# Kernel tuning notes

Measured on AMD Instinct MI355X. Metric: run time of the kernel, lower is better.

The kernel has to match this reference:

```python
import jax, jax.numpy as jnp
import numpy as np

DIM = 16
NUM_SPECIES = 10
CUTOFF = 5.0
NUM_CONVS = 3
N_ATM = 131072
N_BND = 1048576
N_ANG = 2097152
N_GRAPHS = 256
PI = 3.141592653589793


def _bessel(x, end, num_basis):
    # Sinusoidal (Bessel) radial basis on (0, end]. x: [E] -> [E, num_basis]
    xx = x[:, None] + 1e-5
    n = jnp.arange(1, num_basis + 1, dtype=x.dtype)
    return jnp.sqrt(2.0 / end) * jnp.sin(n * PI * xx / end) / xx


def _gaussian(x, start, end, num_basis):
    centers = jnp.linspace(start, end, num_basis).astype(x.dtype)
    gamma = 1.0 / (centers[1] - centers[0])
    return jnp.exp(-(gamma * (x[:, None] - centers)) ** 2)


def _ln(x, g, b):
    mu = jnp.mean(x, -1, keepdims=True)
    var = jnp.var(x, -1, keepdims=True)
    return (x - mu) * jax.lax.rsqrt(var + 1e-5) * g + b


def _embed(feat, W1, b1, W2, b2, g, b):
    # MLP([in, dim, dim], SiLU) + LayerNorm
    h = jax.nn.silu(feat @ W1 + b1)
    return _ln(h @ W2 + b2, g, b)


def _egconv(x, e, src, dst, W, bvec, lnp):
    # Edge-gated graph convolution (ALIGNN layer).
    # W: [5, D, D] = (W_src, W_dst, W_e, W_self, W_nbr); bvec: [2, D]; lnp: [2, 2, D]
    z = x[src] @ W[0] + x[dst] @ W[1] + e @ W[2] + bvec[0]  # [E, D]
    sigma = jax.nn.sigmoid(z)
    msg = sigma * (x[src] @ W[4])
    num = jax.ops.segment_sum(msg, dst, num_segments=x.shape[0])
    den = jax.ops.segment_sum(sigma, dst, num_segments=x.shape[0])
    x_new = x + jax.nn.silu(_ln(x @ W[3] + bvec[1] + num / (den + 1e-5), lnp[0, 0], lnp[0, 1]))
    e_new = e + jax.nn.silu(_ln(z, lnp[1, 0], lnp[1, 1]))
    return x_new, e_new


def _forward(x_atm, x_bnd, x_ang, mask_dih_ang, edge_index_G, edge_index_A, x_atm_batch,
             forcepair, enc_W1, enc_b1, enc_W2, enc_b2, enc_ln_g, enc_ln_b,
             conv_W, conv_b, conv_ln, l1_W, l1_b, l2_W, l2_b):
    # ---- Encoder ----
    # atom species one-hot, zero-padded from NUM_SPECIES to DIM columns (extra W rows unused)
    atm_feat = jax.nn.one_hot(x_atm, DIM, dtype=enc_W1.dtype)
    h_atm = _embed(atm_feat, enc_W1[0], enc_b1[0], enc_W2[0], enc_b2[0], enc_ln_g[0], enc_ln_b[0])
    h_bnd = _embed(_bessel(x_bnd, CUTOFF, DIM), enc_W1[1], enc_b1[1], enc_W2[1], enc_b2[1], enc_ln_g[1], enc_ln_b[1])
    h_ang_b = _embed(_gaussian(x_ang, 0.0, PI, DIM), enc_W1[2], enc_b1[2], enc_W2[2], enc_b2[2], enc_ln_g[2], enc_ln_b[2])
    h_ang_d = _embed(_gaussian(x_ang, -PI, PI, DIM), enc_W1[3], enc_b1[3], enc_W2[3], enc_b2[3], enc_ln_g[3], enc_ln_b[3])
    h_ang = jnp.where(mask_dih_ang[:, None], h_ang_d, h_ang_b)  # dihedral=True branch
    # ---- Processor: interleaved line-graph / atom-graph edge-gated convs ----
    srcA, dstA = edge_index_A[0], edge_index_A[1]
    srcG, dstG = edge_index_G[0], edge_index_G[1]
    for c in range(NUM_CONVS):
        h_bnd, h_ang = _egconv(h_bnd, h_ang, srcA, dstA, conv_W[c, 0], conv_b[c, 0], conv_ln[c, 0])
        h_atm, h_bnd = _egconv(h_atm, h_bnd, srcG, dstG, conv_W[c, 1], conv_b[c, 1], conv_ln[c, 1])
    # ---- Decoder: sum-pool atoms per graph ----
    h_pooled = jax.ops.segment_sum(h_atm, x_atm_batch, num_segments=N_GRAPHS)  # [G, D]
    # ---- Head ----
    x = jnp.concatenate([h_pooled, forcepair.reshape(N_GRAPHS, 2)], axis=-1)  # [G, D+2]
    x = jax.nn.leaky_relu(x @ l1_W + l1_b, negative_slope=0.01)
    return x @ l2_W + l2_b  # [G, 1]


def setup_inputs() -> dict:
    key = jax.random.key(0)
    ks = jax.random.split(key, 16)
    f32 = jnp.float32
    s = 0.25
    inp = {}
    inp["x_atm"] = jax.random.randint(ks[0], (N_ATM,), 0, NUM_SPECIES)
    inp["x_bnd"] = jax.random.uniform(ks[1], (N_BND,), f32, 0.5, CUTOFF)
    inp["x_ang"] = jax.random.uniform(ks[2], (N_ANG,), f32, -PI, PI)
    inp["mask_dih_ang"] = jax.random.randint(ks[3], (N_ANG,), 0, 2).astype(bool)
    inp["edge_index_G"] = jax.random.randint(ks[4], (2, N_BND), 0, N_ATM)
    inp["edge_index_A"] = jax.random.randint(ks[5], (2, N_ANG), 0, N_BND)
    inp["x_atm_batch"] = jnp.sort(jax.random.randint(ks[6], (N_ATM,), 0, N_GRAPHS))
    inp["forcepair"] = jax.random.normal(ks[7], (N_GRAPHS * 2,), f32)
    inp["enc_W1"] = jax.random.normal(ks[8], (4, DIM, DIM), f32) * s
    inp["enc_b1"] = jnp.zeros((4, DIM), f32)
    inp["enc_W2"] = jax.random.normal(ks[9], (4, DIM, DIM), f32) * s
    inp["enc_b2"] = jnp.zeros((4, DIM), f32)
    inp["enc_ln_g"] = jnp.ones((4, DIM), f32)
    inp["enc_ln_b"] = jnp.zeros((4, DIM), f32)
    inp["conv_W"] = jax.random.normal(ks[10], (NUM_CONVS, 2, 5, DIM, DIM), f32) * s
    inp["conv_b"] = jnp.zeros((NUM_CONVS, 2, 2, DIM), f32)
    inp["conv_ln"] = jnp.stack([jnp.ones((NUM_CONVS, 2, 2, DIM), f32), jnp.zeros((NUM_CONVS, 2, 2, DIM), f32)], axis=3)  # [C,2,2(node/edge? no: gamma/beta at axis 3)] -> [C,2,2,2,D]
    inp["l1_W"] = jax.random.normal(ks[11], (DIM + 2, DIM), f32) * s
    inp["l1_b"] = jnp.zeros((DIM,), f32)
    inp["l2_W"] = jax.random.normal(ks[12], (DIM, 1), f32) * s
    inp["l2_b"] = jnp.zeros((1,), f32)
    return inp


def reference(x_atm, x_bnd, x_ang, mask_dih_ang, edge_index_G, edge_index_A, x_atm_batch,
              forcepair, enc_W1, enc_b1, enc_W2, enc_b2, enc_ln_g, enc_ln_b,
              conv_W, conv_b, conv_ln, l1_W, l1_b, l2_W, l2_b):
    return _forward(x_atm, x_bnd, x_ang, mask_dih_ang, edge_index_G, edge_index_A, x_atm_batch,
                    forcepair, enc_W1, enc_b1, enc_W2, enc_b2, enc_ln_g, enc_ln_b,
                    conv_W, conv_b, conv_ln, l1_W, l1_b, l2_W, l2_b)
```

## Files before the change

kernel.cpp:

```cpp
#include <hip/hip_runtime.h>
#include <hip/hip_bf16.h>

#define N_ATM 131072
#define N_BND 1048576
#define N_ANG 2097152
#define N_GRAPHS 256
#define D_SPLIT (N_BND / 2)
#define CAP_SLOTS (N_ANG / 2 + 16384)
#define PI_F 3.14159265358979323846f

typedef __hip_bfloat16 bf16;

__device__ __forceinline__ int clampi(int v, int lo, int hi) {
    return v < lo ? lo : (v > hi ? hi : v);
}
__device__ __forceinline__ float b2f(bf16 v) { return __bfloat162float(v); }
__device__ __forceinline__ float sigmoidf_(float x) { return 1.0f / (1.0f + __expf(-x)); }
__device__ __forceinline__ float siluf_(float x) { return x / (1.0f + __expf(-x)); }

__device__ __forceinline__ float loadF(const void* p, long long i, int isbf) {
    return isbf ? b2f(((const bf16*)p)[i]) : ((const float*)p)[i];
}
__device__ __forceinline__ float bfbits2f(unsigned lo16) {
    union { unsigned u; float f; } c; c.u = lo16 << 16; return c.f;
}
__device__ __forceinline__ unsigned f2bfbits(float f) {
    union { float f; unsigned u; } c; c.f = f;
    unsigned u = c.u + 0x7FFFu + ((c.u >> 16) & 1u);
    return u >> 16;
}

__device__ __forceinline__ void load16b(const bf16* p, float* r) {
    uint4 a = ((const uint4*)p)[0];
    uint4 b = ((const uint4*)p)[1];
    unsigned w[8] = {a.x, a.y, a.z, a.w, b.x, b.y, b.z, b.w};
#pragma unroll
    for (int i = 0; i < 8; i++) {
        r[2*i] = bfbits2f(w[i] & 0xFFFFu);
        union { unsigned u; float f; } c; c.u = w[i] & 0xFFFF0000u;
        r[2*i+1] = c.f;
    }
}
__device__ __forceinline__ void store16b(bf16* p, const float* r) {
    unsigned w[8];
#pragma unroll
    for (int i = 0; i < 8; i++)
        w[i] = f2bfbits(r[2*i]) | (f2bfbits(r[2*i+1]) << 16);
    ((uint4*)p)[0] = make_uint4(w[0], w[1], w[2], w[3]);
    ((uint4*)p)[1] = make_uint4(w[4], w[5], w[6], w[7]);
}

__global__ void __launch_bounds__(256) k_zero_int(int* __restrict__ p, int n) {
    int i = blockIdx.x * 256 + threadIdx.x;
    if (i < n) p[i] = 0;
}

__global__ void __launch_bounds__(256) k_detect(const void* lng, const unsigned* __restrict__ mask,
                                                int* flags) {
    int i = blockIdx.x * 256 + threadIdx.x;
    if (i == 0) flags[0] = (*(const unsigned*)lng == 0x3F803F80u) ? 1 : 0;
    int bad = 0;
    for (int j = i; j < 512 * 1024; j += 512 * 256)
        if (mask[j] > 1u) bad = 1;
    if (bad) atomicOr(&flags[1], 1);
}

__global__ void k_cvt_any(const void* __restrict__ src, float* __restrict__ dst, int n,
                          const int* __restrict__ flags) {
    int i = blockIdx.x * blockDim.x + threadIdx.x;
    if (i < n) dst[i] = loadF(src, i, flags[0]);
}

__global__ void __launch_bounds__(256) k_count(const int* __restrict__ dst, int* __restrict__ cnt,
                                               int E, int n) {
    int i = blockIdx.x * 256 + threadIdx.x;
    if (i >= E) return;
    atomicAdd(&cnt[clampi(dst[i], 0, n - 1)], 1);
}
__global__ void __launch_bounds__(256) k_scan_local(const int* __restrict__ cnt, int* __restrict__ ofs,
                                                    int* __restrict__ bsum, int n) {
    __shared__ int s[256];
    int t = threadIdx.x, i = blockIdx.x * 256 + t;
    int v = (i < n) ? cnt[i] : 0;
    s[t] = v; __syncthreads();
    for (int o = 1; o < 256; o <<= 1) {
        int add = (t >= o) ? s[t - o] : 0;
        __syncthreads();
        s[t] += add;
        __syncthreads();
    }
    if (i < n) ofs[i] = s[t] - v;
    if (t == 255) bsum[blockIdx.x] = s[255];
}
__global__ void __launch_bounds__(256) k_scan_bsum(int* __restrict__ bsum, int nb) {
    __shared__ int s[256];
    __shared__ int run;
    int t = threadIdx.x;
    if (t == 0) run = 0;
    __syncthreads();
    for (int base = 0; base < nb; base += 256) {
        int i = base + t;
        int v = (i < nb) ? bsum[i] : 0;
        s[t] = v; __syncthreads();
        for (int o = 1; o < 256; o <<= 1) {
            int add = (t >= o) ? s[t - o] : 0;
            __syncthreads();
            s[t] += add;
            __syncthreads();
        }
        if (i < nb) bsum[i] = run + s[t] - v;
        __syncthreads();
        if (t == 0) run += s[255];
        __syncthreads();
    }
}
__global__ void __launch_bounds__(256) k_scan_add(int* __restrict__ ofs, const int* __restrict__ bsum,
                                                  int* __restrict__ cursor, int n) {
    int i = blockIdx.x * 256 + threadIdx.x;
    if (i < n) { int v = ofs[i] + bsum[blockIdx.x]; ofs[i] = v; cursor[i] = v; }
}
__global__ void __launch_bounds__(256) k_scatter_line(
    const int* __restrict__ src, const int* __restrict__ dst, int* __restrict__ cur,
    int* __restrict__ srcP, int* __restrict__ dstP, int* __restrict__ pos, int E, int n)
{
    int i = blockIdx.x * 256 + threadIdx.x;
    if (i >= E) return;
    int d = clampi(dst[i], 0, n - 1);
    int s = clampi(src[i], 0, n - 1);
    int p = clampi(atomicAdd(&cur[d], 1), 0, E - 1);
    srcP[p] = s; dstP[p] = d; pos[i] = p;
}
__global__ void __launch_bounds__(256) k_scatter_pos(
    const int* __restrict__ dst, int* __restrict__ cur, int* __restrict__ pos, int E, int n)
{
    int i = blockIdx.x * 256 + threadIdx.x;
    if (i >= E) return;
    int d = clampi(dst[i], 0, n - 1);
    pos[i] = clampi(atomicAdd(&cur[d], 1), 0, E - 1);
}

__global__ void __launch_bounds__(256) k_enc_atm(
    const int* __restrict__ sp_in,
    const void* W1, const void* b1, const void* W2, const void* b2,
    const void* g, const void* be, const int* __restrict__ flags,
    bf16* __restrict__ out)
{
    __shared__ float sW1[256], sW2[256], sb1[16], sb2[16], sg[16], sbe[16];
    int t = threadIdx.x, isbf = flags[0];
    sW1[t] = loadF(W1, t, isbf); sW2[t] = loadF(W2, t, isbf);
    if (t < 16) { sb1[t]=loadF(b1,t,isbf); sb2[t]=loadF(b2,t,isbf); sg[t]=loadF(g,t,isbf); sbe[t]=loadF(be,t,isbf); }
    __syncthreads();
    int i = blockIdx.x * 256 + t;
    if (i >= N_ATM) return;
    int sp = clampi(sp_in[i], 0, 15);
    float h[16];
#pragma unroll
    for (int j = 0; j < 16; j++) h[j] = siluf_(sW1[sp * 16 + j] + sb1[j]);
    float o[16]; float mu = 0.f;
#pragma unroll
    for (int j = 0; j < 16; j++) {
        float a = sb2[j];
#pragma unroll
        for (int k = 0; k < 16; k++) a += h[k] * sW2[k * 16 + j];
        o[j] = a; mu += a;
    }
    mu *= (1.f / 16.f);
    float var = 0.f;
#pragma unroll
    for (int j = 0; j < 16; j++) { float d = o[j] - mu; var += d * d; }
    var *= (1.f / 16.f);
    float r = rsqrtf(var + 1e-5f);
    float ov[16];
#pragma unroll
    for (int j = 0; j < 16; j++) ov[j] = (o[j] - mu) * r * sg[j] + sbe[j];
    store16b(out + (long long)i * 16, ov);
}

__global__ void __launch_bounds__(256) k_enc_bnd(
    const void* __restrict__ xb,
    const void* W1, const void* b1, const void* W2, const void* b2,
    const void* g, const void* be, const int* __restrict__ flags,
    bf16* __restrict__ out)
{
    __shared__ float sW1[256], sW2[256], sb1[16], sb2[16], sg[16], sbe[16];
    int t = threadIdx.x, isbf = flags[0];
    sW1[t] = loadF(W1, 256 + t, isbf); sW2[t] = loadF(W2, 256 + t, isbf);
    if (t < 16) { sb1[t]=loadF(b1,16+t,isbf); sb2[t]=loadF(b2,16+t,isbf); sg[t]=loadF(g,16+t,isbf); sbe[t]=loadF(be,16+t,isbf); }
    __syncthreads();
    int i = blockIdx.x * 256 + t;
    if (i >= N_BND) return;
    float x = loadF(xb, i, isbf) + 1e-5f;
    const float c = 0.6324555320336759f;
    float inv = c / x;
    float feat[16];
#pragma unroll
    for (int k = 0; k < 16; k++) feat[k] = __sinf((float)(k + 1) * PI_F * x * 0.2f) * inv;
    float h[16];
#pragma unroll
    for (int j = 0; j < 16; j++) {
        float a = sb1[j];
#pragma unroll
        for (int k = 0; k < 16; k++) a += feat[k] * sW1[k * 16 + j];
        h[j] = siluf_(a);
    }
    float o[16]; float mu = 0.f;
#pragma unroll
    for (int j = 0; j < 16; j++) {
        float a = sb2[j];
#pragma unroll
        for (int k = 0; k < 16; k++) a += h[k] * sW2[k * 16 + j];
        o[j] = a; mu += a;
    }
    mu *= (1.f / 16.f);
    float var = 0.f;
#pragma unroll
    for (int j = 0; j < 16; j++) { float d = o[j] - mu; var += d * d; }
    var *= (1.f / 16.f);
    float r = rsqrtf(var + 1e-5f);
    float ov[16];
#pragma unroll
    for (int j = 0; j < 16; j++) ov[j] = (o[j] - mu) * r * sg[j] + sbe[j];
    store16b(out + (long long)i * 16, ov);
}

__global__ void __launch_bounds__(256) k_enc_ang(
    const void* __restrict__ xa, const void* __restrict__ mask,
    const void* W1, const void* b1, const void* W2, const void* b2,
    const void* g, const void* be, const int* __restrict__ flags,
    const int* __restrict__ pos, bf16* __restrict__ out)
{
    __shared__ float sW1[512], sW2[512], sb1[32], sb2[32], sg[32], sbe[32];
    int t = threadIdx.x, isbf = flags[0], mbyte = flags[1];
    for (int i = t; i < 512; i += 256) { sW1[i] = loadF(W1, 512 + i, isbf); sW2[i] = loadF(W2, 512 + i, isbf); }
    if (t < 32) { sb1[t]=loadF(b1,32+t,isbf); sb2[t]=loadF(b2,32+t,isbf); sg[t]=loadF(g,32+t,isbf); sbe[t]=loadF(be,32+t,isbf); }
    __syncthreads();
    int i = blockIdx.x * 256 + t;
    if (i >= N_ANG) return;
    int m = mbyte ? (((const unsigned char*)mask)[i] != 0) : (((const int*)mask)[i] != 0);
    float x = loadF(xa, i, isbf);
    float gam = m ? 2.3873241463784303f : 4.7746482927568605f;
    float c0  = m ? -PI_F : 0.0f;
    float dc  = m ? 0.41887902047863906f : 0.20943951023931953f;
    int wo = m * 256, vo = m * 16;
    float feat[16];
#pragma unroll
    for (int k = 0; k < 16; k++) {
        float d = gam * (x - (c0 + (float)k * dc));
        feat[k] = __expf(-d * d);
    }
    float h[16];
#pragma unroll
    for (int j = 0; j < 16; j++) {
        float a = sb1[vo + j];
#pragma unroll
        for (int k = 0; k < 16; k++) a += feat[k] * sW1[wo + k * 16 + j];
        h[j] = siluf_(a);
    }
    float o[16]; float mu = 0.f;
#pragma unroll
    for (int j = 0; j < 16; j++) {
        float a = sb2[vo + j];
#pragma unroll
        for (int k = 0; k < 16; k++) a += h[k] * sW2[wo + k * 16 + j];
        o[j] = a; mu += a;
    }
    mu *= (1.f / 16.f);
    float var = 0.f;
#pragma unroll
    for (int j = 0; j < 16; j++) { float d = o[j] - mu; var += d * d; }
    var *= (1.f / 16.f);
    float r = rsqrtf(var + 1e-5f);
    float ov[16];
#pragma unroll
    for (int j = 0; j < 16; j++) ov[j] = (o[j] - mu) * r * sg[vo + j] + sbe[vo + j];
    store16b(out + (long long)clampi(pos[i], 0, N_ANG - 1) * 16, ov);
}

__device__ __forceinline__ void edge_core(
    const float* xs, const float* xd, const float* ev,
    const float* sW, const float* sB, const float* sLg, const float* sLb,
    float* eo, unsigned* wpk)
{
    float z[16], mm[16];
#pragma unroll
    for (int j = 0; j < 16; j++) { z[j] = sB[j]; mm[j] = 0.f; }
#pragma unroll
    for (int k = 0; k < 16; k++) {
        float a = xs[k], c = xd[k], q = ev[k];
#pragma unroll
        for (int j = 0; j < 16; j++) {
            z[j] += a * sW[k * 16 + j] + c * sW[256 + k * 16 + j] + q * sW[512 + k * 16 + j];
            mm[j] += a * sW[1024 + k * 16 + j];
        }
    }
    float mu = 0.f;
#pragma unroll
    for (int j = 0; j < 16; j++) mu += z[j];
    mu *= (1.f / 16.f);
    float var = 0.f;
#pragma unroll
    for (int j = 0; j < 16; j++) { float dd = z[j] - mu; var += dd * dd; }
    var *= (1.f / 16.f);
    float r = rsqrtf(var + 1e-5f);
#pragma unroll
    for (int j = 0; j < 16; j++)
        eo[j] = ev[j] + siluf_((z[j] - mu) * r * sLg[j] + sLb[j]);
#pragma unroll
    for (int i = 0; i < 8; i++) {
        float a0 = sigmoidf_(z[2*i]);
        float a1 = sigmoidf_(z[2*i+1]);
        wpk[i]     = f2bfbits(a0 * mm[2*i]) | (f2bfbits(a1 * mm[2*i+1]) << 16);
        wpk[8 + i] = f2bfbits(a0)           | (f2bfbits(a1) << 16);
    }
}

__global__ void __launch_bounds__(256) k_econv_side(
    const bf16* __restrict__ x, bf16* __restrict__ e,
    const int* __restrict__ srcP, const int* __restrict__ dstP,
    const float* __restrict__ W, const float* __restrict__ B, const float* __restrict__ L,
    bf16* __restrict__ scratch, int side, int E, int nn)
{
    __shared__ float sW[1280], sB[16], sLg[16], sLb[16];
    int t = threadIdx.x;
    for (int i = t; i < 1280; i += 256) sW[i] = W[i];
    if (t < 16) { sB[t] = B[t]; sLg[t] = L[32 + t]; sLb[t] = L[48 + t]; }
    __syncthreads();
    int p = blockIdx.x * 256 + t;
    if (p >= E) return;
    int d = clampi(dstP[p], 0, nn - 1);
    bool mine = side ? (d >= D_SPLIT) : (d < D_SPLIT);
    if (!mine) return;
    int s = clampi(srcP[p], 0, nn - 1);
    float xs[16], xd[16], ev[16];
    load16b(x + (long long)s * 16, xs);
    load16b(x + (long long)d * 16, xd);
    load16b(e + (long long)p * 16, ev);
    float eo[16]; unsigned wpk[16];
    edge_core(xs, xd, ev, sW, sB, sLg, sLb, eo, wpk);
    store16b(e + (long long)p * 16, eo);
    int slot = side ? (E - 1 - p) : p;
    slot = clampi(slot, 0, CAP_SLOTS - 1);
    uint4* sp4 = (uint4*)(scratch + (long long)slot * 32);
    sp4[0] = make_uint4(wpk[0],  wpk[1],  wpk[2],  wpk[3]);
    sp4[1] = make_uint4(wpk[4],  wpk[5],  wpk[6],  wpk[7]);
    sp4[2] = make_uint4(wpk[8],  wpk[9],  wpk[10], wpk[11]);
    sp4[3] = make_uint4(wpk[12], wpk[13], wpk[14], wpk[15]);
}

__global__ void __launch_bounds__(256) k_econv_nat(
    const bf16* __restrict__ x, bf16* __restrict__ e,
    const int* __restrict__ src, const int* __restrict__ dst, const int* __restrict__ pos,
    const float* __restrict__ W, const float* __restrict__ B, const float* __restrict__ L,
    bf16* __restrict__ scratch, int E, int nn)
{
    __shared__ float sW[1280], sB[16], sLg[16], sLb[16];
    int t = threadIdx.x;
    for (int i = t; i < 1280; i += 256) sW[i] = W[i];
    if (t < 16) { sB[t] = B[t]; sLg[t] = L[32 + t]; sLb[t] = L[48 + t]; }
    __syncthreads();
    int i = blockIdx.x * 256 + t;
    if (i >= E) return;
    int s = clampi(src[i], 0, nn - 1);
    int d = clampi(dst[i], 0, nn - 1);
    float xs[16], xd[16], ev[16];
    load16b(x + (long long)s * 16, xs);
    load16b(x + (long long)d * 16, xd);
    load16b(e + (long long)i * 16, ev);
    float eo[16]; unsigned wpk[16];
    edge_core(xs, xd, ev, sW, sB, sLg, sLb, eo, wpk);
    store16b(e + (long long)i * 16, eo);
    int slot = clampi(pos[i], 0, E - 1);
    uint4* sp4 = (uint4*)(scratch + (long long)slot * 32);
    sp4[0] = make_uint4(wpk[0],  wpk[1],  wpk[2],  wpk[3]);
    sp4[1] = make_uint4(wpk[4],  wpk[5],  wpk[6],  wpk[7]);
    sp4[2] = make_uint4(wpk[8],  wpk[9],  wpk[10], wpk[11]);
    sp4[3] = make_uint4(wpk[12], wpk[13], wpk[14], wpk[15]);
}

__global__ void __launch_bounds__(256) k_nconv(
    const bf16* __restrict__ xo, bf16* __restrict__ xn,
    const int* __restrict__ ofs, const int* __restrict__ endo,
    const float* __restrict__ W, const float* __restrict__ B, const float* __restrict__ L,
    const bf16* __restrict__ scratch, int mulp, int addc,
    int dlo, int dhi, int Emax, int cap)
{
    __shared__ float sW[256], sB[16], sLg[16], sLb[16];
    int t = threadIdx.x;
    sW[t] = W[768 + t];
    if (t < 16) { sB[t] = B[16 + t]; sLg[t] = L[t]; sLb[t] = L[16 + t]; }
    __syncthreads();
    int d = dlo + blockIdx.x * 256 + t;
    if (d >= dhi) return;
    float xv[16];
    load16b(xo + (long long)d * 16, xv);
    float num[16], den[16];
#pragma unroll
    for (int j = 0; j < 16; j++) { num[j] = 0.f; den[j] = 0.f; }
    int p0 = clampi(ofs[d], 0, Emax);
    int p1 = clampi(endo[d], p0, Emax);
    for (int p = p0; p < p1; p++) {
        int idx = clampi(mulp * p + addc, 0, cap - 1);
        const uint4* q = (const uint4*)(scratch + (long long)idx * 32);
        uint4 q0 = q[0], q1 = q[1], q2 = q[2], q3 = q[3];
        unsigned w[16] = {q0.x,q0.y,q0.z,q0.w, q1.x,q1.y,q1.z,q1.w,
                          q2.x,q2.y,q2.z,q2.w, q3.x,q3.y,q3.z,q3.w};
#pragma unroll
        for (int i = 0; i < 8; i++) {
            num[2*i]   += bfbits2f(w[i] & 0xFFFFu);
            num[2*i+1] += bfbits2f(w[i] >> 16);
            den[2*i]   += bfbits2f(w[8+i] & 0xFFFFu);
            den[2*i+1] += bfbits2f(w[8+i] >> 16);
        }
    }
    float tt[16]; float mu = 0.f;
#pragma unroll
    for (int j = 0; j < 16; j++) {
        float a = sB[j] + num[j] / (den[j] + 1e-5f);
#pragma unroll
        for (int k = 0; k < 16; k++) a += xv[k] * sW[k * 16 + j];
        tt[j] = a; mu += a;
    }
    mu *= (1.f / 16.f);
    float var = 0.f;
#pragma unroll
    for (int j = 0; j < 16; j++) { float dd = tt[j] - mu; var += dd * dd; }
    var *= (1.f / 16.f);
    float r = rsqrtf(var + 1e-5f);
    float ov[16];
#pragma unroll
    for (int j = 0; j < 16; j++)
        ov[j] = xv[j] + siluf_((tt[j] - mu) * r * sLg[j] + sLb[j]);
    store16b(xn + (long long)d * 16, ov);
}

__global__ void __launch_bounds__(256) k_pool2(
    const bf16* __restrict__ h, const int* __restrict__ batch, float* __restrict__ pooled)
{
    int g = blockIdx.x;
    int lo = 0, hi = N_ATM;
    while (lo < hi) { int m = (lo + hi) >> 1; if (batch[m] < g) lo = m + 1; else hi = m; }
    int s0 = lo;
    lo = 0; hi = N_ATM;
    while (lo < hi) { int m = (lo + hi) >> 1; if (batch[m] < g + 1) lo = m + 1; else hi = m; }
    int s1 = lo;
    float acc[16];
#pragma unroll
    for (int j = 0; j < 16; j++) acc[j] = 0.f;
    for (int i = s0 + threadIdx.x; i < s1; i += 256) {
        float v[16];
        load16b(h + (long long)i * 16, v);
#pragma unroll
        for (int j = 0; j < 16; j++) acc[j] += v[j];
    }
#pragma unroll
    for (int j = 0; j < 16; j++)
        for (int o = 32; o > 0; o >>= 1) acc[j] += __shfl_down(acc[j], o, 64);
    __shared__ float red[4][16];
    int wv = threadIdx.x >> 6, ln = threadIdx.x & 63;
    if (ln == 0)
#pragma unroll
        for (int j = 0; j < 16; j++) red[wv][j] = acc[j];
    __syncthreads();
    if (threadIdx.x < 16)
        pooled[g * 16 + threadIdx.x] = red[0][threadIdx.x] + red[1][threadIdx.x]
                                     + red[2][threadIdx.x] + red[3][threadIdx.x];
}

__global__ void __launch_bounds__(256) k_head(
    const float* __restrict__ pooled, const void* __restrict__ fp,
    const void* l1W, const void* l1b, const void* l2W, const void* l2b,
    const int* __restrict__ flags, void* __restrict__ out)
{
    __shared__ float sW[18 * 16], sb[16], s2W[16];
    int t = threadIdx.x, isbf = flags[0];
    for (int i = t; i < 288; i += 256) sW[i] = loadF(l1W, i, isbf);
    if (t < 16) { sb[t] = loadF(l1b, t, isbf); s2W[t] = loadF(l2W, t, isbf); }
    __syncthreads();
    int g = t;
    if (g >= N_GRAPHS) return;
    float in[18];
#pragma unroll
    for (int j = 0; j < 16; j++) in[j] = pooled[g * 16 + j];
    in[16] = loadF(fp, 2 * g, isbf);
    in[17] = loadF(fp, 2 * g + 1, isbf);
    float acc = loadF(l2b, 0, isbf);
#pragma unroll
    for (int j = 0; j < 16; j++) {
        float h = sb[j];
#pragma unroll
        for (int k = 0; k < 18; k++) h += in[k] * sW[k * 16 + j];
        h = (h > 0.f) ? h : 0.01f * h;
        acc += h * s2W[j];
    }
    if (isbf) ((bf16*)out)[g] = __float2bfloat16(acc);
    else      ((float*)out)[g] = acc;
}

extern "C" void kernel_launch(void* const* d_in, const int* in_sizes, int n_in,
                              void* d_out, int out_size, void* d_ws, size_t ws_size,
                              hipStream_t stream) {
    const int*  x_atm = (const int*)d_in[0];
    const void* x_bnd = d_in[1];
    const void* x_ang = d_in[2];
    const void* mask  = d_in[3];
    const int*  eiG   = (const int*)d_in[4];
    const int*  eiA   = (const int*)d_in[5];
    const int*  batch = (const int*)d_in[6];
    const void* fp    = d_in[7];
    const void* eW1 = d_in[8],  *eb1 = d_in[9],  *eW2 = d_in[10], *eb2 = d_in[11];
    const void* elg = d_in[12], *elb = d_in[13];
    const void* convW = d_in[14], *convB = d_in[15], *convLN = d_in[16];
    const void* l1W = d_in[17], *l1b = d_in[18], *l2W = d_in[19], *l2b = d_in[20];

    const size_t NA16 = (size_t)N_ATM * 16;
    const size_t NB16 = (size_t)N_BND * 16;
    const size_t NG16 = (size_t)N_ANG * 16;

    char* p = (char*)d_ws;
    int*   flags  = (int*)p;   p += 256;
    float* cw     = (float*)p; p += 7680 * 4;
    float* cb     = (float*)p; p += 192 * 4;
    float* cln    = (float*)p; p += 384 * 4;
    float* pooled = (float*)p; p += 4096 * 4;
    int*   bsum   = (int*)p;   p += 4096 * 4;
    int*   cntB   = (int*)p;   p += (size_t)N_BND * 4;
    int*   ofsB   = (int*)p;   p += (size_t)N_BND * 4;
    int*   srcB   = (int*)p;   p += (size_t)N_ANG * 4;
    int*   dstB   = (int*)p;   p += (size_t)N_ANG * 4;
    int*   cntA   = (int*)p;   p += (size_t)N_ATM * 4;
    int*   ofsA   = (int*)p;   p += (size_t)N_ATM * 4;
    int*   posG   = (int*)p;   p += (size_t)N_BND * 4;
    bf16*  h_atm  = (bf16*)p;  p += NA16 * 2;
    bf16*  h_bndX = (bf16*)p;  p += NB16 * 2;
    bf16*  h_bndY = (bf16*)p;  p += NB16 * 2;
    bf16*  h_ang  = (bf16*)p;  p += NG16 * 2;
    int*   posB    = (int*)p;
    bf16*  scratch = (bf16*)p;

    k_zero_int<<<1, 64, 0, stream>>>(flags, 64);
    k_detect<<<512, 256, 0, stream>>>(elg, (const unsigned*)mask, flags);
    k_cvt_any<<<30, 256, 0, stream>>>(convW, cw, 7680, flags);
    k_cvt_any<<<1, 256, 0, stream>>>(convB, cb, 192, flags);
    k_cvt_any<<<2, 256, 0, stream>>>(convLN, cln, 384, flags);

    k_zero_int<<<N_BND / 256, 256, 0, stream>>>(cntB, N_BND);
    k_count<<<N_ANG / 256, 256, 0, stream>>>(eiA + N_ANG, cntB, N_ANG, N_BND);
    k_scan_local<<<N_BND / 256, 256, 0, stream>>>(cntB, ofsB, bsum, N_BND);
    k_scan_bsum<<<1, 256, 0, stream>>>(bsum, N_BND / 256);
    k_scan_add<<<N_BND / 256, 256, 0, stream>>>(ofsB, bsum, cntB, N_BND);
    k_scatter_line<<<N_ANG / 256, 256, 0, stream>>>(eiA, eiA + N_ANG, cntB, srcB, dstB, posB,
                                                    N_ANG, N_BND);
    k_zero_int<<<N_ATM / 256, 256, 0, stream>>>(cntA, N_ATM);
    k_count<<<N_BND / 256, 256, 0, stream>>>(eiG + N_BND, cntA, N_BND, N_ATM);
    k_scan_local<<<N_ATM / 256, 256, 0, stream>>>(cntA, ofsA, bsum, N_ATM);
    k_scan_bsum<<<1, 256, 0, stream>>>(bsum, N_ATM / 256);
    k_scan_add<<<N_ATM / 256, 256, 0, stream>>>(ofsA, bsum, cntA, N_ATM);
    k_scatter_pos<<<N_BND / 256, 256, 0, stream>>>(eiG + N_BND, cntA, posG, N_BND, N_ATM);

    k_enc_atm<<<N_ATM / 256, 256, 0, stream>>>(x_atm, eW1, eb1, eW2, eb2, elg, elb, flags, h_atm);
    k_enc_bnd<<<N_BND / 256, 256, 0, stream>>>(x_bnd, eW1, eb1, eW2, eb2, elg, elb, flags, h_bndX);
    k_enc_ang<<<N_ANG / 256, 256, 0, stream>>>(x_ang, mask, eW1, eb1, eW2, eb2, elg, elb, flags,
                                               posB, h_ang);

    bf16* X = h_bndX;
    bf16* Y = h_bndY;
    for (int c = 0; c < 3; c++) {
        const float* Wl = cw + (size_t)(c * 2 + 0) * 1280;
        const float* Bl = cb + (size_t)(c * 2 + 0) * 32;
        const float* Ll = cln + (size_t)(c * 2 + 0) * 64;
        k_econv_side<<<N_ANG / 256, 256, 0, stream>>>(X, h_ang, srcB, dstB, Wl, Bl, Ll,
                                                      scratch, 0, N_ANG, N_BND);
        k_nconv<<<D_SPLIT / 256, 256, 0, stream>>>(X, Y, ofsB, cntB, Wl, Bl, Ll,
                                                   scratch, 1, 0,
                                                   0, D_SPLIT, N_ANG, CAP_SLOTS);
        k_econv_side<<<N_ANG / 256, 256, 0, stream>>>(X, h_ang, srcB, dstB, Wl, Bl, Ll,
                                                      scratch, 1, N_ANG, N_BND);
        k_nconv<<<(N_BND - D_SPLIT) / 256, 256, 0, stream>>>(X, Y, ofsB, cntB, Wl, Bl, Ll,
                                                             scratch, -1, N_ANG - 1,
                                                             D_SPLIT, N_BND, N_ANG, CAP_SLOTS);
        const float* Wa = cw + (size_t)(c * 2 + 1) * 1280;
        const float* Ba = cb + (size_t)(c * 2 + 1) * 32;
        const float* La = cln + (size_t)(c * 2 + 1) * 64;
        k_econv_nat<<<N_BND / 256, 256, 0, stream>>>(h_atm, Y, eiG, eiG + N_BND, posG,
                                                     Wa, Ba, La, scratch, N_BND, N_ATM);
        k_nconv<<<N_ATM / 256, 256, 0, stream>>>(h_atm, h_atm, ofsA, cntA, Wa, Ba, La,
                                                 scratch, 1, 0,
                                                 0, N_ATM, N_BND, N_BND);
        bf16* tmp = X; X = Y; Y = tmp;
    }

    k_pool2<<<N_GRAPHS, 256, 0, stream>>>(h_atm, batch, pooled);
    k_head<<<1, 256, 0, stream>>>(pooled, fp, l1W, l1b, l2W, l2b, flags, d_out);
}
```

Measured before the change: 2.576 ms.

## Unify edge conv kernels, quantize sigmoid gates to u8, drop bond ping-pong buffers

Replaces the two-pass side-split line-graph edge conv with one kernel that reads the edge indices in their original order and scatters its outputs to CSR-sorted slots. The per-edge scratch shrinks from 64 to 48 bytes by storing the sigmoid gate denominators as 8-bit fixed point instead of bf16. Node conv updates in place using ofs[d+1] as the segment end, which drops the cursor arrays and the double-buffered bond features. This cuts scratch traffic and kernel launches, but loses precision in the gate sums and relies on in-place node updates being safe.

```diff
diff --git a/kernel.cpp b/kernel.cpp
--- a/kernel.cpp
+++ b/kernel.cpp
@@ -5,8 +5,6 @@
 #define N_BND 1048576
 #define N_ANG 2097152
 #define N_GRAPHS 256
-#define D_SPLIT (N_BND / 2)
-#define CAP_SLOTS (N_ANG / 2 + 16384)
 #define PI_F 3.14159265358979323846f
 
 typedef __hip_bfloat16 bf16;
@@ -119,17 +117,6 @@
     int i = blockIdx.x * 256 + threadIdx.x;
     if (i < n) { int v = ofs[i] + bsum[blockIdx.x]; ofs[i] = v; cursor[i] = v; }
 }
-__global__ void __launch_bounds__(256) k_scatter_line(
-    const int* __restrict__ src, const int* __restrict__ dst, int* __restrict__ cur,
-    int* __restrict__ srcP, int* __restrict__ dstP, int* __restrict__ pos, int E, int n)
-{
-    int i = blockIdx.x * 256 + threadIdx.x;
-    if (i >= E) return;
-    int d = clampi(dst[i], 0, n - 1);
-    int s = clampi(src[i], 0, n - 1);
-    int p = clampi(atomicAdd(&cur[d], 1), 0, E - 1);
-    srcP[p] = s; dstP[p] = d; pos[i] = p;
-}
 __global__ void __launch_bounds__(256) k_scatter_pos(
     const int* __restrict__ dst, int* __restrict__ cur, int* __restrict__ pos, int E, int n)
 {
@@ -279,7 +266,7 @@
 __device__ __forceinline__ void edge_core(
     const float* xs, const float* xd, const float* ev,
     const float* sW, const float* sB, const float* sLg, const float* sLb,
-    float* eo, unsigned* wpk)
+    float* eo, unsigned* wmm, unsigned* wsg)
 {
     float z[16], mm[16];
 #pragma unroll
@@ -305,111 +292,89 @@
 #pragma unroll
     for (int j = 0; j < 16; j++)
         eo[j] = ev[j] + siluf_((z[j] - mu) * r * sLg[j] + sLb[j]);
-#pragma unroll
-    for (int i = 0; i < 8; i++) {
-        float a0 = sigmoidf_(z[2*i]);
-        float a1 = sigmoidf_(z[2*i+1]);
-        wpk[i]     = f2bfbits(a0 * mm[2*i]) | (f2bfbits(a1 * mm[2*i+1]) << 16);
-        wpk[8 + i] = f2bfbits(a0)           | (f2bfbits(a1) << 16);
-    }
-}
-
-__global__ void __launch_bounds__(256) k_econv_side(
+    float sg[16];
+#pragma unroll
+    for (int j = 0; j < 16; j++) sg[j] = sigmoidf_(z[j]);
+#pragma unroll
+    for (int i = 0; i < 8; i++)
+        wmm[i] = f2bfbits(sg[2*i] * mm[2*i]) | (f2bfbits(sg[2*i+1] * mm[2*i+1]) << 16);
+#pragma unroll
+    for (int q = 0; q < 4; q++) {
+        unsigned u0 = (unsigned)clampi((int)(sg[4*q+0] * 255.f + 0.5f), 1, 255);
+        unsigned u1 = (unsigned)clampi((int)(sg[4*q+1] * 255.f + 0.5f), 1, 255);
+        unsigned u2 = (unsigned)clampi((int)(sg[4*q+2] * 255.f + 0.5f), 1, 255);
+        unsigned u3 = (unsigned)clampi((int)(sg[4*q+3] * 255.f + 0.5f), 1, 255);
+        wsg[q] = u0 | (u1 << 8) | (u2 << 16) | (u3 << 24);
+    }
+}
+
+__global__ void __launch_bounds__(256) k_econv(
     const bf16* __restrict__ x, bf16* __restrict__ e,
-    const int* __restrict__ srcP, const int* __restrict__ dstP,
+    const int* __restrict__ src, const int* __restrict__ dst, const int* __restrict__ pos,
     const float* __restrict__ W, const float* __restrict__ B, const float* __restrict__ L,
-    bf16* __restrict__ scratch, int side, int E, int nn)
+    bf16* __restrict__ scratch48, int eAtSlot, int E, int nn)
 {
     __shared__ float sW[1280], sB[16], sLg[16], sLb[16];
     int t = threadIdx.x;
     for (int i = t; i < 1280; i += 256) sW[i] = W[i];
     if (t < 16) { sB[t] = B[t]; sLg[t] = L[32 + t]; sLb[t] = L[48 + t]; }
     __syncthreads();
-    int p = blockIdx.x * 256 + t;
-    if (p >= E) return;
-    int d = clampi(dstP[p], 0, nn - 1);
-    bool mine = side ? (d >= D_SPLIT) : (d < D_SPLIT);
-    if (!mine) return;
-    int s = clampi(srcP[p], 0, nn - 1);
-    float xs[16], xd[16], ev[16];
-    load16b(x + (long long)s * 16, xs);
-    load16b(x + (long long)d * 16, xd);
-    load16b(e + (long long)p * 16, ev);
-    float eo[16]; unsigned wpk[16];
-    edge_core(xs, xd, ev, sW, sB, sLg, sLb, eo, wpk);
-    store16b(e + (long long)p * 16, eo);
-    int slot = side ? (E - 1 - p) : p;
-    slot = clampi(slot, 0, CAP_SLOTS - 1);
-    uint4* sp4 = (uint4*)(scratch + (long long)slot * 32);
-    sp4[0] = make_uint4(wpk[0],  wpk[1],  wpk[2],  wpk[3]);
-    sp4[1] = make_uint4(wpk[4],  wpk[5],  wpk[6],  wpk[7]);
-    sp4[2] = make_uint4(wpk[8],  wpk[9],  wpk[10], wpk[11]);
-    sp4[3] = make_uint4(wpk[12], wpk[13], wpk[14], wpk[15]);
-}
-
-__global__ void __launch_bounds__(256) k_econv_nat(
-    const bf16* __restrict__ x, bf16* __restrict__ e,
-    const int* __restrict__ src, const int* __restrict__ dst, const int* __restrict__ pos,
-    const float* __restrict__ W, const float* __restrict__ B, const float* __restrict__ L,
-    bf16* __restrict__ scratch, int E, int nn)
-{
-    __shared__ float sW[1280], sB[16], sLg[16], sLb[16];
-    int t = threadIdx.x;
-    for (int i = t; i < 1280; i += 256) sW[i] = W[i];
-    if (t < 16) { sB[t] = B[t]; sLg[t] = L[32 + t]; sLb[t] = L[48 + t]; }
-    __syncthreads();
     int i = blockIdx.x * 256 + t;
     if (i >= E) return;
     int s = clampi(src[i], 0, nn - 1);
     int d = clampi(dst[i], 0, nn - 1);
+    int slot = clampi(pos[i], 0, E - 1);
+    long long erow = eAtSlot ? (long long)slot : (long long)i;
     float xs[16], xd[16], ev[16];
     load16b(x + (long long)s * 16, xs);
     load16b(x + (long long)d * 16, xd);
-    load16b(e + (long long)i * 16, ev);
-    float eo[16]; unsigned wpk[16];
-    edge_core(xs, xd, ev, sW, sB, sLg, sLb, eo, wpk);
-    store16b(e + (long long)i * 16, eo);
-    int slot = clampi(pos[i], 0, E - 1);
-    uint4* sp4 = (uint4*)(scratch + (long long)slot * 32);
-    sp4[0] = make_uint4(wpk[0],  wpk[1],  wpk[2],  wpk[3]);
-    sp4[1] = make_uint4(wpk[4],  wpk[5],  wpk[6],  wpk[7]);
-    sp4[2] = make_uint4(wpk[8],  wpk[9],  wpk[10], wpk[11]);
-    sp4[3] = make_uint4(wpk[12], wpk[13], wpk[14], wpk[15]);
+    load16b(e + erow * 16, ev);
+    float eo[16]; unsigned wmm[8], wsg[4];
+    edge_core(xs, xd, ev, sW, sB, sLg, sLb, eo, wmm, wsg);
+    store16b(e + erow * 16, eo);
+    uint4* sp = (uint4*)(scratch48 + (long long)slot * 24);
+    sp[0] = make_uint4(wmm[0], wmm[1], wmm[2], wmm[3]);
+    sp[1] = make_uint4(wmm[4], wmm[5], wmm[6], wmm[7]);
+    sp[2] = make_uint4(wsg[0], wsg[1], wsg[2], wsg[3]);
 }
 
 __global__ void __launch_bounds__(256) k_nconv(
-    const bf16* __restrict__ xo, bf16* __restrict__ xn,
-    const int* __restrict__ ofs, const int* __restrict__ endo,
+    bf16* __restrict__ x,
+    const int* __restrict__ ofs,
     const float* __restrict__ W, const float* __restrict__ B, const float* __restrict__ L,
-    const bf16* __restrict__ scratch, int mulp, int addc,
-    int dlo, int dhi, int Emax, int cap)
+    const bf16* __restrict__ scratch48, int n, int E)
 {
     __shared__ float sW[256], sB[16], sLg[16], sLb[16];
     int t = threadIdx.x;
     sW[t] = W[768 + t];
     if (t < 16) { sB[t] = B[16 + t]; sLg[t] = L[t]; sLb[t] = L[16 + t]; }
     __syncthreads();
-    int d = dlo + blockIdx.x * 256 + t;
-    if (d >= dhi) return;
+    int d = blockIdx.x * 256 + t;
+    if (d >= n) return;
     float xv[16];
-    load16b(xo + (long long)d * 16, xv);
+    load16b(x + (long long)d * 16, xv);
     float num[16], den[16];
 #pragma unroll
     for (int j = 0; j < 16; j++) { num[j] = 0.f; den[j] = 0.f; }
-    int p0 = clampi(ofs[d], 0, Emax);
-    int p1 = clampi(endo[d], p0, Emax);
+    int p0 = clampi(ofs[d], 0, E);
+    int p1 = (d + 1 < n) ? clampi(ofs[d + 1], p0, E) : E;
+    const float inv255 = 1.f / 255.f;
     for (int p = p0; p < p1; p++) {
-        int idx = clampi(mulp * p + addc, 0, cap - 1);
-        const uint4* q = (const uint4*)(scratch + (long long)idx * 32);
-        uint4 q0 = q[0], q1 = q[1], q2 = q[2], q3 = q[3];
-        unsigned w[16] = {q0.x,q0.y,q0.z,q0.w, q1.x,q1.y,q1.z,q1.w,
-                          q2.x,q2.y,q2.z,q2.w, q3.x,q3.y,q3.z,q3.w};
+        const uint4* q = (const uint4*)(scratch48 + (long long)p * 24);
+        uint4 a = q[0], b = q[1], c = q[2];
+        unsigned wm[8] = {a.x, a.y, a.z, a.w, b.x, b.y, b.z, b.w};
 #pragma unroll
         for (int i = 0; i < 8; i++) {
-            num[2*i]   += bfbits2f(w[i] & 0xFFFFu);
-            num[2*i+1] += bfbits2f(w[i] >> 16);
-            den[2*i]   += bfbits2f(w[8+i] & 0xFFFFu);
-            den[2*i+1] += bfbits2f(w[8+i] >> 16);
+            num[2*i]   += bfbits2f(wm[i] & 0xFFFFu);
+            num[2*i+1] += bfbits2f(wm[i] >> 16);
+        }
+        unsigned ws[4] = {c.x, c.y, c.z, c.w};
+#pragma unroll
+        for (int qd = 0; qd < 4; qd++) {
+            den[4*qd+0] += (float)( ws[qd]        & 0xFFu) * inv255;
+            den[4*qd+1] += (float)((ws[qd] >> 8 ) & 0xFFu) * inv255;
+            den[4*qd+2] += (float)((ws[qd] >> 16) & 0xFFu) * inv255;
+            den[4*qd+3] += (float)((ws[qd] >> 24) & 0xFFu) * inv255;
         }
     }
     float tt[16]; float mu = 0.f;
@@ -430,7 +395,7 @@
 #pragma unroll
     for (int j = 0; j < 16; j++)
         ov[j] = xv[j] + siluf_((tt[j] - mu) * r * sLg[j] + sLb[j]);
-    store16b(xn + (long long)d * 16, ov);
+    store16b(x + (long long)d * 16, ov);
 }
 
 __global__ void __launch_bounds__(256) k_pool2(
@@ -523,18 +488,15 @@
     float* cln    = (float*)p; p += 384 * 4;
     float* pooled = (float*)p; p += 4096 * 4;
     int*   bsum   = (int*)p;   p += 4096 * 4;
-    int*   cntB   = (int*)p;   p += (size_t)N_BND * 4;
     int*   ofsB   = (int*)p;   p += (size_t)N_BND * 4;
-    int*   srcB   = (int*)p;   p += (size_t)N_ANG * 4;
-    int*   dstB   = (int*)p;   p += (size_t)N_ANG * 4;
-    int*   cntA   = (int*)p;   p += (size_t)N_ATM * 4;
     int*   ofsA   = (int*)p;   p += (size_t)N_ATM * 4;
+    int*   posB   = (int*)p;   p += (size_t)N_ANG * 4;
     int*   posG   = (int*)p;   p += (size_t)N_BND * 4;
     bf16*  h_atm  = (bf16*)p;  p += NA16 * 2;
-    bf16*  h_bndX = (bf16*)p;  p += NB16 * 2;
-    bf16*  h_bndY = (bf16*)p;  p += NB16 * 2;
+    bf16*  h_bnd  = (bf16*)p;  p += NB16 * 2;
     bf16*  h_ang  = (bf16*)p;  p += NG16 * 2;
-    int*   posB    = (int*)p;
+    int*   cntB    = (int*)p;
+    int*   cntA    = (int*)(p + (size_t)N_BND * 4);
     bf16*  scratch = (bf16*)p;
 
     k_zero_int<<<1, 64, 0, stream>>>(flags, 64);
@@ -548,8 +510,7 @@
     k_scan_local<<<N_BND / 256, 256, 0, stream>>>(cntB, ofsB, bsum, N_BND);
     k_scan_bsum<<<1, 256, 0, stream>>>(bsum, N_BND / 256);
     k_scan_add<<<N_BND / 256, 256, 0, stream>>>(ofsB, bsum, cntB, N_BND);
-    k_scatter_line<<<N_ANG / 256, 256, 0, stream>>>(eiA, eiA + N_ANG, cntB, srcB, dstB, posB,
-                                                    N_ANG, N_BND);
+    k_scatter_pos<<<N_ANG / 256, 256, 0, stream>>>(eiA + N_ANG, cntB, posB, N_ANG, N_BND);
     k_zero_int<<<N_ATM / 256, 256, 0, stream>>>(cntA, N_ATM);
     k_count<<<N_BND / 256, 256, 0, stream>>>(eiG + N_BND, cntA, N_BND, N_ATM);
     k_scan_local<<<N_ATM / 256, 256, 0, stream>>>(cntA, ofsA, bsum, N_ATM);
@@ -558,35 +519,24 @@
     k_scatter_pos<<<N_BND / 256, 256, 0, stream>>>(eiG + N_BND, cntA, posG, N_BND, N_ATM);
 
     k_enc_atm<<<N_ATM / 256, 256, 0, stream>>>(x_atm, eW1, eb1, eW2, eb2, elg, elb, flags, h_atm);
-    k_enc_bnd<<<N_BND / 256, 256, 0, stream>>>(x_bnd, eW1, eb1, eW2, eb2, elg, elb, flags, h_bndX);
+    k_enc_bnd<<<N_BND / 256, 256, 0, stream>>>(x_bnd, eW1, eb1, eW2, eb2, elg, elb, flags, h_bnd);
     k_enc_ang<<<N_ANG / 256, 256, 0, stream>>>(x_ang, mask, eW1, eb1, eW2, eb2, elg, elb, flags,
                                                posB, h_ang);
 
-    bf16* X = h_bndX;
-    bf16* Y = h_bndY;
     for (int c = 0; c < 3; c++) {
         const float* Wl = cw + (size_t)(c * 2 + 0) * 1280;
         const float* Bl = cb + (size_t)(c * 2 + 0) * 32;
         const float* Ll = cln + (size_t)(c * 2 + 0) * 64;
-        k_econv_side<<<N_ANG / 256, 256, 0, stream>>>(X, h_ang, srcB, dstB, Wl, Bl, Ll,
-                                                      scratch, 0, N_ANG, N_BND);
-        k_nconv<<<D_SPLIT / 256, 256, 0, stream>>>(X, Y, ofsB, cntB, Wl, Bl, Ll,
-                                                   scratch, 1, 0,
-                                                   0, D_SPLIT, N_ANG, CAP_SLOTS);
-        k_econv_side<<<N_ANG / 256, 256, 0, stream>>>(X, h_ang, srcB, dstB, Wl, Bl, Ll,
-                                                      scratch, 1, N_ANG, N_BND);
-        k_nconv<<<(N_BND - D_SPLIT) / 256, 256, 0, stream>>>(X, Y, ofsB, cntB, Wl, Bl, Ll,
-                                                             scratch, -1, N_ANG - 1,
-                                                             D_SPLIT, N_BND, N_ANG, CAP_SLOTS);
+        k_econv<<<N_ANG / 256, 256, 0, stream>>>(h_bnd, h_ang, eiA, eiA + N_ANG, posB,
+                                                 Wl, Bl, Ll, scratch, 1, N_ANG, N_BND);
+        k_nconv<<<N_BND / 256, 256, 0, stream>>>(h_bnd, ofsB, Wl, Bl, Ll, scratch, N_BND, N_ANG);
+
         const float* Wa = cw + (size_t)(c * 2 + 1) * 1280;
         const float* Ba = cb + (size_t)(c * 2 + 1) * 32;
         const float* La = cln + (size_t)(c * 2 + 1) * 64;
-        k_econv_nat<<<N_BND / 256, 256, 0, stream>>>(h_atm, Y, eiG, eiG + N_BND, posG,
-                                                     Wa, Ba, La, scratch, N_BND, N_ATM);
-        k_nconv<<<N_ATM / 256, 256, 0, stream>>>(h_atm, h_atm, ofsA, cntA, Wa, Ba, La,
-                                                 scratch, 1, 0,
-                                                 0, N_ATM, N_BND, N_BND);
-        bf16* tmp = X; X = Y; Y = tmp;
+        k_econv<<<N_BND / 256, 256, 0, stream>>>(h_atm, h_bnd, eiG, eiG + N_BND, posG,
+                                                 Wa, Ba, La, scratch, 0, N_BND, N_ATM);
+        k_nconv<<<N_ATM / 256, 256, 0, stream>>>(h_atm, ofsA, Wa, Ba, La, scratch, N_ATM, N_BND);
     }
 
     k_pool2<<<N_GRAPHS, 256, 0, stream>>>(h_atm, batch, pooled);
```

Result: slower. 2.633 ms (+2.2%).
